# Kernel tuning notes

Hardware: AMD Instinct MI355X
Metric: run time of the kernel (lower is better)

The kernel has to match this reference:

```python
import jax, jax.numpy as jnp
import numpy as np

N_LEVELS = 9

def _avg_pool_2x2(x):
    # tf.nn.avg_pool2d(ksize=2, strides=2, padding='SAME'); H,W even at every
    # level for H=W=512, so SAME == VALID == simple 2x2 mean.
    b, h, w, c = x.shape
    return x.reshape(b, h // 2, 2, w // 2, 2, c).mean(axis=(2, 4))

def setup_inputs() -> dict:
    key = jax.random.key(0)
    x = jax.random.normal(key, (8, 512, 512, 2), dtype=jnp.float32)
    return {"x": x}

def reference(x):
    B, H, W, C = x.shape
    levels = [x]
    cur = x
    for _ in range(N_LEVELS - 1):
        cur = _avg_pool_2x2(cur)
        levels.append(cur)
    # tf.image.resize bilinear (half-pixel centers, no antialias on upsample)
    # == jax.image.resize method='bilinear' for upscaling.
    ups = [jax.image.resize(lv, (B, H, W, C), method='bilinear') for lv in levels]
    stacked = jnp.concatenate(ups, axis=-1)          # [B, H, W, 9*C]
    stacked = stacked[:, None]                       # [B, 1, H, W, 9*C]
    return jnp.transpose(stacked, (0, 4, 2, 3, 1))   # [B, 9*C, H, W, 1]
```

## Files before the change

### kernel.cpp

```cpp
#include <hip/hip_runtime.h>


#define HWTOT (512 * 512)
#define RW 292

typedef float vfloat4 __attribute__((ext_vector_type(4)));

__constant__ int c_off2[7] = {0, 0, 524288, 655360, 688128, 696320, 698368};

__global__ __launch_bounds__(256) void build_levels_1_6(const float* __restrict__ x,
                                                        float2* __restrict__ pyr,
                                                        float* __restrict__ out) {
  const int b = blockIdx.y;
  const int tx = blockIdx.x & 7, ty = blockIdx.x >> 3;
  const int t = threadIdx.x;

  __shared__ float2 sh1[32 * 32];
  __shared__ float2 sh2[16 * 16];
  __shared__ float2 sh3[8 * 8];
  __shared__ float2 sh4[4 * 4];
  __shared__ float2 sh5[2 * 2];

  {
    const int i = t >> 3;
    const int j0 = (t & 7) << 2;
    const int row0 = ty * 64 + 2 * i;
    const int colx = tx * 64 + 2 * j0;
    const float* r0 = x + (((size_t)(b * 512 + row0)) * 512 + colx) * 2;
    const float* r1 = r0 + 1024;
    float4 a[4], c[4];
    float2 o[4];
#pragma unroll
    for (int k = 0; k < 4; ++k) {
      a[k] = *(const float4*)(r0 + 4 * k);
      c[k] = *(const float4*)(r1 + 4 * k);
      o[k].x = (a[k].x + a[k].z + c[k].x + c[k].z) * 0.25f;
      o[k].y = (a[k].y + a[k].w + c[k].y + c[k].w) * 0.25f;
      sh1[i * 32 + j0 + k] = o[k];
    }
    float2* g = pyr + ((size_t)(b * 256 + ty * 32 + i) * 256 + tx * 32 + j0);
    *(float4*)(g) = make_float4(o[0].x, o[0].y, o[1].x, o[1].y);
    *(float4*)(g + 2) = make_float4(o[2].x, o[2].y, o[3].x, o[3].y);

    const size_t ob = (size_t)(b * 18) * HWTOT + (size_t)row0 * 512 + colx;
    *(vfloat4*)(out + ob)                  = (vfloat4){a[0].x, a[0].z, a[1].x, a[1].z};
    *(vfloat4*)(out + ob + 4)              = (vfloat4){a[2].x, a[2].z, a[3].x, a[3].z};
    *(vfloat4*)(out + ob + 512)            = (vfloat4){c[0].x, c[0].z, c[1].x, c[1].z};
    *(vfloat4*)(out + ob + 512 + 4)        = (vfloat4){c[2].x, c[2].z, c[3].x, c[3].z};
    *(vfloat4*)(out + ob + HWTOT)          = (vfloat4){a[0].y, a[0].w, a[1].y, a[1].w};
    *(vfloat4*)(out + ob + HWTOT + 4)      = (vfloat4){a[2].y, a[2].w, a[3].y, a[3].w};
    *(vfloat4*)(out + ob + HWTOT + 512)    = (vfloat4){c[0].y, c[0].w, c[1].y, c[1].w};
    *(vfloat4*)(out + ob + HWTOT + 512 + 4)= (vfloat4){c[2].y, c[2].w, c[3].y, c[3].w};
  }
  __syncthreads();
  {
    const int i = t >> 4, j = t & 15;
    float2 a = sh1[(2 * i) * 32 + 2 * j], c = sh1[(2 * i) * 32 + 2 * j + 1];
    float2 d = sh1[(2 * i + 1) * 32 + 2 * j], e = sh1[(2 * i + 1) * 32 + 2 * j + 1];
    float2 o = {(a.x + c.x + d.x + e.x) * 0.25f, (a.y + c.y + d.y + e.y) * 0.25f};
    sh2[i * 16 + j] = o;
    pyr[524288 + (size_t)(b * 128 + ty * 16 + i) * 128 + tx * 16 + j] = o;
  }
  __syncthreads();
  if (t < 64) {
    const int i = t >> 3, j = t & 7;
    float2 a = sh2[(2 * i) * 16 + 2 * j], c = sh2[(2 * i) * 16 + 2 * j + 1];
    float2 d = sh2[(2 * i + 1) * 16 + 2 * j], e = sh2[(2 * i + 1) * 16 + 2 * j + 1];
    float2 o = {(a.x + c.x + d.x + e.x) * 0.25f, (a.y + c.y + d.y + e.y) * 0.25f};
    sh3[i * 8 + j] = o;
    pyr[655360 + (size_t)(b * 64 + ty * 8 + i) * 64 + tx * 8 + j] = o;
  }
  __syncthreads();
  if (t < 16) {
    const int i = t >> 2, j = t & 3;
    float2 a = sh3[(2 * i) * 8 + 2 * j], c = sh3[(2 * i) * 8 + 2 * j + 1];
    float2 d = sh3[(2 * i + 1) * 8 + 2 * j], e = sh3[(2 * i + 1) * 8 + 2 * j + 1];
    float2 o = {(a.x + c.x + d.x + e.x) * 0.25f, (a.y + c.y + d.y + e.y) * 0.25f};
    sh4[i * 4 + j] = o;
    pyr[688128 + (size_t)(b * 32 + ty * 4 + i) * 32 + tx * 4 + j] = o;
  }
  __syncthreads();
  if (t < 4) {
    const int i = t >> 1, j = t & 1;
    float2 a = sh4[(2 * i) * 4 + 2 * j], c = sh4[(2 * i) * 4 + 2 * j + 1];
    float2 d = sh4[(2 * i + 1) * 4 + 2 * j], e = sh4[(2 * i + 1) * 4 + 2 * j + 1];
    float2 o = {(a.x + c.x + d.x + e.x) * 0.25f, (a.y + c.y + d.y + e.y) * 0.25f};
    sh5[i * 2 + j] = o;
    pyr[696320 + (size_t)(b * 16 + ty * 2 + i) * 16 + tx * 2 + j] = o;
  }
  __syncthreads();
  if (t == 0) {
    float2 a = sh5[0], c = sh5[1], d = sh5[2], e = sh5[3];
    float2 o = {(a.x + c.x + d.x + e.x) * 0.25f, (a.y + c.y + d.y + e.y) * 0.25f};
    pyr[698368 + (size_t)(b * 8 + ty) * 8 + tx] = o;
  }
}

__global__ __launch_bounds__(256) void upsample_lv(const float2* __restrict__ pyr,
                                                   float* __restrict__ out) {
  const int t = threadIdx.x;
  const int tp = t & 127;
  const int rr0 = t >> 7;
  const int w0pix = tp << 2;
  const int bx = blockIdx.x;
  const int b = blockIdx.y;
  const int lv = blockIdx.z + 1;
  const int S = 512 >> lv;
  const float scale = 1.0f / (float)(1 << lv);

  __shared__ float2 rows[6 * RW + 20];

  const int W = S + 2;
  const int hbase = (int)floorf(((float)(bx << 3) + 0.5f) * scale - 0.5f);

  if (lv == 1) {
#pragma unroll
    for (int r = 0; r < 6; ++r) {
      int sr = hbase + r;
      sr = sr < 0 ? 0 : (sr > S - 1 ? S - 1 : sr);
      const float2* src = pyr + (size_t)b * S * S + (size_t)sr * S;
      for (int c = t; c < W; c += 256) {
        int sc = c - 1;
        sc = sc < 0 ? 0 : (sc > S - 1 ? S - 1 : sc);
        rows[r * RW + c + (c >> 3)] = src[sc];
      }
    }
  } else if (lv <= 6) {
#pragma unroll
    for (int r = 0; r < 6; ++r) {
      int sr = hbase + r;
      sr = sr < 0 ? 0 : (sr > S - 1 ? S - 1 : sr);
      const float2* src = pyr + c_off2[lv] + (size_t)b * S * S + (size_t)sr * S;
      if (t < W) {
        int sc = t - 1;
        sc = sc < 0 ? 0 : (sc > S - 1 ? S - 1 : sc);
        rows[r * RW + t] = src[sc];
      }
    }
  } else {
    float2* img7 = rows + 6 * RW;
    float2* img8 = img7 + 16;
    const float2* l6 = pyr + 698368 + (size_t)b * 64;
    if (t < 16) {
      const int i = t >> 2, j = t & 3;
      float2 a = l6[(2 * i) * 8 + 2 * j], c = l6[(2 * i) * 8 + 2 * j + 1];
      float2 d = l6[(2 * i + 1) * 8 + 2 * j], e = l6[(2 * i + 1) * 8 + 2 * j + 1];
      img7[t] = {(a.x + c.x + d.x + e.x) * 0.25f, (a.y + c.y + d.y + e.y) * 0.25f};
    }
    __syncthreads();
    if (lv == 8 && t < 4) {
      const int i = t >> 1, j = t & 1;
      float2 a = img7[(2 * i) * 4 + 2 * j], c = img7[(2 * i) * 4 + 2 * j + 1];
      float2 d = img7[(2 * i + 1) * 4 + 2 * j], e = img7[(2 * i + 1) * 4 + 2 * j + 1];
      img8[t] = {(a.x + c.x + d.x + e.x) * 0.25f, (a.y + c.y + d.y + e.y) * 0.25f};
    }
    __syncthreads();
    const float2* img = (lv == 7) ? img7 : img8;
    if (t < 6 * W) {
      int r = t / W;
      int c = t - r * W;
      int sr = hbase + r;
      sr = sr < 0 ? 0 : (sr > S - 1 ? S - 1 : sr);
      int sc = c - 1;
      sc = sc < 0 ? 0 : (sc > S - 1 ? S - 1 : sc);
      rows[r * RW + c] = img[sr * S + sc];
    }
  }
  __syncthreads();

  const size_t obase0 =
      (size_t)(b * 18 + 2 * lv) * HWTOT + (size_t)((bx << 3) + rr0) * 512 + w0pix;

  if (lv == 1) {
    const int e0 = tp << 1;
    const int i0 = e0 + (e0 >> 3);
    const int i1 = (e0 + 1) + ((e0 + 1) >> 3);
    const int i2 = (e0 + 2) + ((e0 + 2) >> 3);
    const int i3 = (e0 + 3) + ((e0 + 3) >> 3);
#pragma unroll
    for (int dr2 = 0; dr2 < 4; ++dr2) {
      const int rr = rr0 + 2 * dr2;
      const int d0 = (rr + 1) >> 1;
      const float fh = (rr & 1) ? 0.25f : 0.75f;
      const float wy0 = 1.0f - fh;
      const float2* R0 = rows + d0 * RW;
      const float2* R1 = R0 + RW;
      float2 p0 = R0[i0], p1 = R0[i1], p2 = R0[i2], p3 = R0[i3];
      float2 q0 = R1[i0], q1 = R1[i1], q2 = R1[i2], q3 = R1[i3];
      float hx0 = p0.x * 0.25f + p1.x * 0.75f, hy0 = p0.y * 0.25f + p1.y * 0.75f;
      float hx1 = p1.x * 0.75f + p2.x * 0.25f, hy1 = p1.y * 0.75f + p2.y * 0.25f;
      float hx2 = p1.x * 0.25f + p2.x * 0.75f, hy2 = p1.y * 0.25f + p2.y * 0.75f;
      float hx3 = p2.x * 0.75f + p3.x * 0.25f, hy3 = p2.y * 0.75f + p3.y * 0.25f;
      float gx0 = q0.x * 0.25f + q1.x * 0.75f, gy0 = q0.y * 0.25f + q1.y * 0.75f;
      float gx1 = q1.x * 0.75f + q2.x * 0.25f, gy1 = q1.y * 0.75f + q2.y * 0.25f;
      float gx2 = q1.x * 0.25f + q2.x * 0.75f, gy2 = q1.y * 0.25f + q2.y * 0.75f;
      float gx3 = q2.x * 0.75f + q3.x * 0.25f, gy3 = q2.y * 0.75f + q3.y * 0.25f;
      const size_t ob = obase0 + (size_t)dr2 * 1024;
      *(vfloat4*)(out + ob) = (vfloat4){hx0 * wy0 + gx0 * fh, hx1 * wy0 + gx1 * fh,
                                        hx2 * wy0 + gx2 * fh, hx3 * wy0 + gx3 * fh};
      *(vfloat4*)(out + ob + HWTOT) = (vfloat4){hy0 * wy0 + gy0 * fh, hy1 * wy0 + gy1 * fh,
                                                hy2 * wy0 + gy2 * fh, hy3 * wy0 + gy3 * fh};
    }
    return;
  }

  int w0l[4];
  float fw[4];
#pragma unroll
  for (int k = 0; k < 4; ++k) {
    float sw = ((float)(w0pix + k) + 0.5f) * scale - 0.5f;
    float f = floorf(sw);
    fw[k] = sw - f;
    w0l[k] = (int)f + 1;
  }
#pragma unroll
  for (int dr2 = 0; dr2 < 4; ++dr2) {
    const int rr = rr0 + 2 * dr2;
    const int h = (bx << 3) + rr;
    float shf = ((float)h + 0.5f) * scale - 0.5f;
    float f0 = floorf(shf);
    float fh = shf - f0;
    int d0 = (int)f0 - hbase;
    const float2* R0 = rows + d0 * RW;
    const float2* R1 = R0 + RW;
    const float wy0 = 1.0f - fh;
    float o0[4], o1[4];
#pragma unroll
    for (int k = 0; k < 4; ++k) {
      float2 v00 = R0[w0l[k]], v01 = R0[w0l[k] + 1];
      float2 v10 = R1[w0l[k]], v11 = R1[w0l[k] + 1];
      float wx0 = 1.0f - fw[k];
      float tx_ = v00.x * wx0 + v01.x * fw[k];
      float bx_ = v10.x * wx0 + v11.x * fw[k];
      float ty_ = v00.y * wx0 + v01.y * fw[k];
      float by_ = v10.y * wx0 + v11.y * fw[k];
      o0[k] = tx_ * wy0 + bx_ * fh;
      o1[k] = ty_ * wy0 + by_ * fh;
    }
    const size_t ob = obase0 + (size_t)dr2 * 1024;
    *(vfloat4*)(out + ob) = (vfloat4){o0[0], o0[1], o0[2], o0[3]};
    *(vfloat4*)(out + ob + HWTOT) = (vfloat4){o1[0], o1[1], o1[2], o1[3]};
  }
}

extern "C" void kernel_launch(void* const* d_in, const int* in_sizes, int n_in,
                              void* d_out, int out_size, void* d_ws, size_t ws_size,
                              hipStream_t stream) {
  const float* x = (const float*)d_in[0];
  float* out = (float*)d_out;
  float2* pyr = (float2*)d_ws;

  build_levels_1_6<<<dim3(64, 8), 256, 0, stream>>>(x, pyr, out);
  upsample_lv<<<dim3(64, 8, 8), 256, 0, stream>>>(pyr, out);
}
```

Measured before the change: 164.7 us.

## Fuse level-1 upsample into pyramid build kernel with haloed shared tile

```diff
diff --git a/kernel.cpp b/kernel.cpp
--- a/kernel.cpp
+++ b/kernel.cpp
@@ -2,61 +2,90 @@
 
 
 #define HWTOT (512 * 512)
-#define RW 292
+#define SW 40
+#define RW 132
 
 typedef float vfloat4 __attribute__((ext_vector_type(4)));
 
 __constant__ int c_off2[7] = {0, 0, 524288, 655360, 688128, 696320, 698368};
 
-__global__ __launch_bounds__(256) void build_levels_1_6(const float* __restrict__ x,
-                                                        float2* __restrict__ pyr,
-                                                        float* __restrict__ out) {
+__global__ __launch_bounds__(512) void build_all(const float* __restrict__ x,
+                                                 float2* __restrict__ pyr,
+                                                 float* __restrict__ out) {
   const int b = blockIdx.y;
   const int tx = blockIdx.x & 7, ty = blockIdx.x >> 3;
   const int t = threadIdx.x;
 
-  __shared__ float2 sh1[32 * 32];
+  __shared__ float2 sh1[34 * SW];
   __shared__ float2 sh2[16 * 16];
   __shared__ float2 sh3[8 * 8];
   __shared__ float2 sh4[4 * 4];
   __shared__ float2 sh5[2 * 2];
 
+  for (int idx = t; idx < 34 * 34; idx += 512) {
+    const int jw = idx / 34;
+    const int iw = idx - jw * 34;
+    int jl = ty * 32 + jw - 1;
+    jl = jl < 0 ? 0 : (jl > 255 ? 255 : jl);
+    int il = tx * 32 + iw - 1;
+    il = il < 0 ? 0 : (il > 255 ? 255 : il);
+    const float* p0 = x + ((size_t)(b * 512 + 2 * jl) * 512 + 2 * il) * 2;
+    float4 a = *(const float4*)p0;
+    float4 c = *(const float4*)(p0 + 1024);
+    sh1[jw * SW + iw + (iw >> 3)] = {(a.x + a.z + c.x + c.z) * 0.25f,
+                                     (a.y + a.w + c.y + c.w) * 0.25f};
+    if (jw >= 1 && jw <= 32 && iw >= 1 && iw <= 32) {
+      const int xr = 2 * jl, xc = 2 * il;
+      const size_t ob = (size_t)(b * 18) * HWTOT + (size_t)xr * 512 + xc;
+      *(float2*)(out + ob) = {a.x, a.z};
+      *(float2*)(out + ob + 512) = {c.x, c.z};
+      *(float2*)(out + ob + HWTOT) = {a.y, a.w};
+      *(float2*)(out + ob + HWTOT + 512) = {c.y, c.w};
+    }
+  }
+  __syncthreads();
+
   {
-    const int i = t >> 3;
-    const int j0 = (t & 7) << 2;
-    const int row0 = ty * 64 + 2 * i;
-    const int colx = tx * 64 + 2 * j0;
-    const float* r0 = x + (((size_t)(b * 512 + row0)) * 512 + colx) * 2;
-    const float* r1 = r0 + 1024;
-    float4 a[4], c[4];
-    float2 o[4];
-#pragma unroll
-    for (int k = 0; k < 4; ++k) {
-      a[k] = *(const float4*)(r0 + 4 * k);
-      c[k] = *(const float4*)(r1 + 4 * k);
-      o[k].x = (a[k].x + a[k].z + c[k].x + c[k].z) * 0.25f;
-      o[k].y = (a[k].y + a[k].w + c[k].y + c[k].w) * 0.25f;
-      sh1[i * 32 + j0 + k] = o[k];
-    }
-    float2* g = pyr + ((size_t)(b * 256 + ty * 32 + i) * 256 + tx * 32 + j0);
-    *(float4*)(g) = make_float4(o[0].x, o[0].y, o[1].x, o[1].y);
-    *(float4*)(g + 2) = make_float4(o[2].x, o[2].y, o[3].x, o[3].y);
-
-    const size_t ob = (size_t)(b * 18) * HWTOT + (size_t)row0 * 512 + colx;
-    *(vfloat4*)(out + ob)                  = (vfloat4){a[0].x, a[0].z, a[1].x, a[1].z};
-    *(vfloat4*)(out + ob + 4)              = (vfloat4){a[2].x, a[2].z, a[3].x, a[3].z};
-    *(vfloat4*)(out + ob + 512)            = (vfloat4){c[0].x, c[0].z, c[1].x, c[1].z};
-    *(vfloat4*)(out + ob + 512 + 4)        = (vfloat4){c[2].x, c[2].z, c[3].x, c[3].z};
-    *(vfloat4*)(out + ob + HWTOT)          = (vfloat4){a[0].y, a[0].w, a[1].y, a[1].w};
-    *(vfloat4*)(out + ob + HWTOT + 4)      = (vfloat4){a[2].y, a[2].w, a[3].y, a[3].w};
-    *(vfloat4*)(out + ob + HWTOT + 512)    = (vfloat4){c[0].y, c[0].w, c[1].y, c[1].w};
-    *(vfloat4*)(out + ob + HWTOT + 512 + 4)= (vfloat4){c[2].y, c[2].w, c[3].y, c[3].w};
-  }
-  __syncthreads();
-  {
+    const int g = t & 15;
+    const int r0_ = t >> 4;
+    const int e0 = g << 1;
+    const int i0 = e0 + (e0 >> 3);
+    const int i1 = (e0 + 1) + ((e0 + 1) >> 3);
+    const int i2 = (e0 + 2) + ((e0 + 2) >> 3);
+    const int i3 = (e0 + 3) + ((e0 + 3) >> 3);
+#pragma unroll
+    for (int pass = 0; pass < 2; ++pass) {
+      const int R = r0_ + pass * 32;
+      const int wr = ((R - 1) >> 1) + 1;
+      const float fh = (R & 1) ? 0.25f : 0.75f;
+      const float wy0 = 1.0f - fh;
+      const float2* P = sh1 + wr * SW;
+      const float2* Q = P + SW;
+      float2 p0 = P[i0], p1 = P[i1], p2 = P[i2], p3 = P[i3];
+      float2 q0 = Q[i0], q1 = Q[i1], q2 = Q[i2], q3 = Q[i3];
+      float hx0 = p0.x * 0.25f + p1.x * 0.75f, hy0 = p0.y * 0.25f + p1.y * 0.75f;
+      float hx1 = p1.x * 0.75f + p2.x * 0.25f, hy1 = p1.y * 0.75f + p2.y * 0.25f;
+      float hx2 = p1.x * 0.25f + p2.x * 0.75f, hy2 = p1.y * 0.25f + p2.y * 0.75f;
+      float hx3 = p2.x * 0.75f + p3.x * 0.25f, hy3 = p2.y * 0.75f + p3.y * 0.25f;
+      float gx0 = q0.x * 0.25f + q1.x * 0.75f, gy0 = q0.y * 0.25f + q1.y * 0.75f;
+      float gx1 = q1.x * 0.75f + q2.x * 0.25f, gy1 = q1.y * 0.75f + q2.y * 0.25f;
+      float gx2 = q1.x * 0.25f + q2.x * 0.75f, gy2 = q1.y * 0.25f + q2.y * 0.75f;
+      float gx3 = q2.x * 0.75f + q3.x * 0.25f, gy3 = q2.y * 0.75f + q3.y * 0.25f;
+      const size_t ob =
+          (size_t)(b * 18 + 2) * HWTOT + (size_t)(ty * 64 + R) * 512 + tx * 64 + 4 * g;
+      *(vfloat4*)(out + ob) = (vfloat4){hx0 * wy0 + gx0 * fh, hx1 * wy0 + gx1 * fh,
+                                        hx2 * wy0 + gx2 * fh, hx3 * wy0 + gx3 * fh};
+      *(vfloat4*)(out + ob + HWTOT) = (vfloat4){hy0 * wy0 + gy0 * fh, hy1 * wy0 + gy1 * fh,
+                                                hy2 * wy0 + gy2 * fh, hy3 * wy0 + gy3 * fh};
+    }
+  }
+
+  if (t < 256) {
     const int i = t >> 4, j = t & 15;
-    float2 a = sh1[(2 * i) * 32 + 2 * j], c = sh1[(2 * i) * 32 + 2 * j + 1];
-    float2 d = sh1[(2 * i + 1) * 32 + 2 * j], e = sh1[(2 * i + 1) * 32 + 2 * j + 1];
+    const int ca = (2 * j + 1) + ((2 * j + 1) >> 3);
+    const int cb = (2 * j + 2) + ((2 * j + 2) >> 3);
+    float2 a = sh1[(2 * i + 1) * SW + ca], c = sh1[(2 * i + 1) * SW + cb];
+    float2 d = sh1[(2 * i + 2) * SW + ca], e = sh1[(2 * i + 2) * SW + cb];
     float2 o = {(a.x + c.x + d.x + e.x) * 0.25f, (a.y + c.y + d.y + e.y) * 0.25f};
     sh2[i * 16 + j] = o;
     pyr[524288 + (size_t)(b * 128 + ty * 16 + i) * 128 + tx * 16 + j] = o;
@@ -104,7 +133,7 @@
   const int w0pix = tp << 2;
   const int bx = blockIdx.x;
   const int b = blockIdx.y;
-  const int lv = blockIdx.z + 1;
+  const int lv = blockIdx.z + 2;
   const int S = 512 >> lv;
   const float scale = 1.0f / (float)(1 << lv);
 
@@ -113,19 +142,7 @@
   const int W = S + 2;
   const int hbase = (int)floorf(((float)(bx << 3) + 0.5f) * scale - 0.5f);
 
-  if (lv == 1) {
-#pragma unroll
-    for (int r = 0; r < 6; ++r) {
-      int sr = hbase + r;
-      sr = sr < 0 ? 0 : (sr > S - 1 ? S - 1 : sr);
-      const float2* src = pyr + (size_t)b * S * S + (size_t)sr * S;
-      for (int c = t; c < W; c += 256) {
-        int sc = c - 1;
-        sc = sc < 0 ? 0 : (sc > S - 1 ? S - 1 : sc);
-        rows[r * RW + c + (c >> 3)] = src[sc];
-      }
-    }
-  } else if (lv <= 6) {
+  if (lv <= 6) {
 #pragma unroll
     for (int r = 0; r < 6; ++r) {
       int sr = hbase + r;
@@ -170,39 +187,6 @@
 
   const size_t obase0 =
       (size_t)(b * 18 + 2 * lv) * HWTOT + (size_t)((bx << 3) + rr0) * 512 + w0pix;
-
-  if (lv == 1) {
-    const int e0 = tp << 1;
-    const int i0 = e0 + (e0 >> 3);
-    const int i1 = (e0 + 1) + ((e0 + 1) >> 3);
-    const int i2 = (e0 + 2) + ((e0 + 2) >> 3);
-    const int i3 = (e0 + 3) + ((e0 + 3) >> 3);
-#pragma unroll
-    for (int dr2 = 0; dr2 < 4; ++dr2) {
-      const int rr = rr0 + 2 * dr2;
-      const int d0 = (rr + 1) >> 1;
-      const float fh = (rr & 1) ? 0.25f : 0.75f;
-      const float wy0 = 1.0f - fh;
-      const float2* R0 = rows + d0 * RW;
-      const float2* R1 = R0 + RW;
-      float2 p0 = R0[i0], p1 = R0[i1], p2 = R0[i2], p3 = R0[i3];
-      float2 q0 = R1[i0], q1 = R1[i1], q2 = R1[i2], q3 = R1[i3];
-      float hx0 = p0.x * 0.25f + p1.x * 0.75f, hy0 = p0.y * 0.25f + p1.y * 0.75f;
-      float hx1 = p1.x * 0.75f + p2.x * 0.25f, hy1 = p1.y * 0.75f + p2.y * 0.25f;
-      float hx2 = p1.x * 0.25f + p2.x * 0.75f, hy2 = p1.y * 0.25f + p2.y * 0.75f;
-      float hx3 = p2.x * 0.75f + p3.x * 0.25f, hy3 = p2.y * 0.75f + p3.y * 0.25f;
-      float gx0 = q0.x * 0.25f + q1.x * 0.75f, gy0 = q0.y * 0.25f + q1.y * 0.75f;
-      float gx1 = q1.x * 0.75f + q2.x * 0.25f, gy1 = q1.y * 0.75f + q2.y * 0.25f;
-      float gx2 = q1.x * 0.25f + q2.x * 0.75f, gy2 = q1.y * 0.25f + q2.y * 0.75f;
-      float gx3 = q2.x * 0.75f + q3.x * 0.25f, gy3 = q2.y * 0.75f + q3.y * 0.25f;
-      const size_t ob = obase0 + (size_t)dr2 * 1024;
-      *(vfloat4*)(out + ob) = (vfloat4){hx0 * wy0 + gx0 * fh, hx1 * wy0 + gx1 * fh,
-                                        hx2 * wy0 + gx2 * fh, hx3 * wy0 + gx3 * fh};
-      *(vfloat4*)(out + ob + HWTOT) = (vfloat4){hy0 * wy0 + gy0 * fh, hy1 * wy0 + gy1 * fh,
-                                                hy2 * wy0 + gy2 * fh, hy3 * wy0 + gy3 * fh};
-    }
-    return;
-  }
 
   int w0l[4];
   float fw[4];
@@ -250,6 +234,6 @@
   float* out = (float*)d_out;
   float2* pyr = (float2*)d_ws;
 
-  build_levels_1_6<<<dim3(64, 8), 256, 0, stream>>>(x, pyr, out);
-  upsample_lv<<<dim3(64, 8, 8), 256, 0, stream>>>(pyr, out);
+  build_all<<<dim3(64, 8), 512, 0, stream>>>(x, pyr, out);
+  upsample_lv<<<dim3(64, 8, 7), 256, 0, stream>>>(pyr, out);
 }
```

After: 165.1 us. No clear change (+0.2%).
